# Performance work log

Measured on AMD Instinct MI355X. Metric: run time of the kernel, lower is better.

The kernel has to match this reference:

```python
import jax, jax.numpy as jnp
import numpy as np

N_GAS_NETS = 76  # 29 h2o + 13 o3 + 9 co2 + 3 n2o + 9 ch4 + 13 uniform
N_CHANNELS = 29
N_IN = 2   # (temperature, pressure)
H = 64     # hidden width per n_hidden=[64,64]

# gas index (into composition[0..5]) for each of the 76 stacked nets
COMP_IDX = jnp.asarray(np.repeat(np.arange(6), [29, 13, 9, 3, 9, 13]))

# sparse per-channel combine (hard-coded in the original forward)
H2O_IDX = jnp.asarray([0,1,2,3,4,5,6,3,4,9,10,11,12,13,14,15,16,17,18,19,20,21,22,23,24,25,26,27,28])
O3_CH  = jnp.asarray([0,1,2,17,18,19,20,21,22,25,26,27,28])
CO2_CH = jnp.asarray([0,1,2,5,6,9,10,13,14])
N2O_CH = jnp.asarray([0,1,2])
CH4_CH = jnp.asarray([0,1,2,3,4,7,8,11,12])
U_CH   = jnp.asarray([0,1,2,15,16,17,18,19,20,21,22,27,28])


def setup_inputs() -> dict:
    key = jax.random.key(0)
    ks = jax.random.split(key, 10)
    N = 32768
    t_p = jax.random.normal(ks[0], (N, N_IN), dtype=jnp.float32)
    composition = jax.random.uniform(ks[1], (8, N, 1), dtype=jnp.float32)
    s1 = 1.0 / np.sqrt(N_IN)
    s2 = 1.0 / np.sqrt(H)
    W1 = jax.random.normal(ks[2], (N_GAS_NETS, N_IN, H), dtype=jnp.float32) * s1
    b1 = jnp.zeros((N_GAS_NETS, H), dtype=jnp.float32)
    W2 = jax.random.normal(ks[3], (N_GAS_NETS, H, H), dtype=jnp.float32) * s2
    b2 = jnp.zeros((N_GAS_NETS, H), dtype=jnp.float32)
    Wout = jax.random.normal(ks[4], (N_GAS_NETS, H, 1), dtype=jnp.float32) * s2
    bout = jnp.zeros((N_GAS_NETS, 1), dtype=jnp.float32)
    ke_lw = jax.random.uniform(ks[5], (N_CHANNELS, 1), dtype=jnp.float32)
    ke_iw = jax.random.uniform(ks[6], (N_CHANNELS, 1), dtype=jnp.float32)
    return {"t_p": t_p, "composition": composition, "W1": W1, "b1": b1,
            "W2": W2, "b2": b2, "Wout": Wout, "bout": bout,
            "ke_lw": ke_lw, "ke_iw": ke_iw}


def reference(t_p, composition, W1, b1, W2, b2, Wout, bout, ke_lw, ke_iw):
    # Batched evaluation of all 76 tiny DenseFFN experts on the shared t_p input.
    h = jax.nn.relu(jnp.einsum('ni,gih->gnh', t_p, W1) + b1[:, None, :])   # [76,N,H]
    h = jax.nn.relu(jnp.einsum('gnh,ghk->gnk', h, W2) + b2[:, None, :])    # [76,N,H]
    ke = jax.nn.relu(jnp.einsum('gnh,gho->gno', h, Wout) + bout[:, None, :])  # [76,N,1]

    # tau_gas[gas] = ke * composition[gas_index]
    tau_all = ke * composition[COMP_IDX]  # [76,N,1]
    h2o = tau_all[0:29]
    o3 = tau_all[29:42]
    co2 = tau_all[42:51]
    n2o = tau_all[51:54]
    ch4 = tau_all[54:63]
    u = tau_all[63:76]

    # hard-coded sparse per-channel sum
    tau_gases = h2o[H2O_IDX]                      # [29,N,1]
    tau_gases = tau_gases.at[O3_CH].add(o3)
    tau_gases = tau_gases.at[CO2_CH].add(co2)
    tau_gases = tau_gases.at[N2O_CH].add(n2o)
    tau_gases = tau_gases.at[CH4_CH].add(ch4)
    tau_gases = tau_gases.at[U_CH].add(u)

    tau_lw = ke_lw[:, None, :] * composition[6]   # [29,N,1]
    tau_iw = ke_iw[:, None, :] * composition[7]   # [29,N,1]
    return (tau_gases, tau_lw, tau_iw)
```

## Files before the change

### kernel.cpp

```cpp
#include <hip/hip_runtime.h>

#define NPTS 32768

typedef _Float16 f16;
typedef _Float16 f16x2 __attribute__((ext_vector_type(2)));
typedef _Float16 f16x8 __attribute__((ext_vector_type(8)));
typedef float f32x2 __attribute__((ext_vector_type(2)));
typedef float f32x4 __attribute__((ext_vector_type(4)));
typedef unsigned int u32x4 __attribute__((ext_vector_type(4)));

union U16 { u32x4 u; f32x4 f; f16x2 h2[4]; f16x8 h8; };

static __device__ __forceinline__ f16x2 pk_fma(f16x2 a, f16x2 b, f16x2 c) {
  return __builtin_elementwise_fma(a, b, c);
}
static __device__ __forceinline__ f16x2 pk_relu(f16x2 a) {
  f16x2 z = {(f16)0.f, (f16)0.f};
  return __builtin_elementwise_max(a, z);
}
static __device__ __forceinline__ f16x2 pk_cvt(float a, float b) {
  return __builtin_bit_cast(f16x2, __builtin_amdgcn_cvt_pkrtz(a, b));
}

__device__ const unsigned char G_T[74] = {
  0,0,0,0,0,0,0, 0,0,0,0,0,0,0,0,0,0,0,0,0,0,0,0,0,0,0,0,
  1,1,1,1,1,1,1,1,1,1,1,1,1,
  2,2,2,2,2,2,2,2,2,
  3,3,3,
  4,4,4,4,4,4,4,4,4,
  5,5,5,5,5,5,5,5,5,5,5,5,5
};
__device__ const unsigned char G_C1[74] = {
  0,1,2,3,4,5,6, 9,10,11,12,13,14,15,16,17,18,19,20,21,22,23,24,25,26,27,28,
  0,1,2,17,18,19,20,21,22,25,26,27,28,
  0,1,2,5,6,9,10,13,14,
  0,1,2,
  0,1,2,3,4,7,8,11,12,
  0,1,2,15,16,17,18,19,20,21,22,27,28
};
__device__ const unsigned char G_C2[74] = {
  255,255,255,7,8,255,255, 255,255,255,255,255,255,255,255,255,255,255,255,
  255,255,255,255,255,255,255,255,
  255,255,255,255,255,255,255,255,255,255,255,255,255,
  255,255,255,255,255,255,255,255,255,
  255,255,255,
  255,255,255,255,255,255,255,255,255,
  255,255,255,255,255,255,255,255,255,255,255,255,255
};

#define NSLOT 22

__global__ __launch_bounds__(64) void k0w_pack(
    const float* __restrict__ W1, const float* __restrict__ b1,
    const float* __restrict__ W2, const float* __restrict__ b2,
    const float* __restrict__ Wout, u32x4* __restrict__ pack)
{
  const int gi   = blockIdx.x;
  const int lane = threadIdx.x;
  const int l15  = lane & 15;
  const int quad = lane >> 4;
  const int g    = gi + (gi >= 7 ? 2 : 0);

  const float* W2g = W2 + g * 4096;
  const float* W1g = W1 + g * 128;
  const float* b1g = b1 + g * 64;
  u32x4* dst = pack + gi * NSLOT * 64 + lane;

  #pragma unroll
  for (int mt = 0; mt < 4; ++mt)
    #pragma unroll
    for (int ks = 0; ks < 2; ++ks) {
      U16 u;
      #pragma unroll
      for (int j = 0; j < 4; ++j) {
        const float* s = W2g + (ks * 32 + quad * 8 + 2 * j) * 64 + mt * 16 + l15;
        u.h2[j] = pk_cvt(s[0], s[64]);
      }
      dst[(mt * 2 + ks) * 64] = u.u;
    }
  #pragma unroll
  for (int ks = 0; ks < 2; ++ks) {
    U16 a, b, c;
    #pragma unroll
    for (int j = 0; j < 4; ++j) {
      int h = ks * 32 + quad * 8 + 2 * j;
      a.h2[j] = pk_cvt(W1g[h],      W1g[h + 1]);
      b.h2[j] = pk_cvt(W1g[64 + h], W1g[64 + h + 1]);
      c.h2[j] = pk_cvt(b1g[h],      b1g[h + 1]);
    }
    dst[(8 + ks) * 64]  = a.u;
    dst[(10 + ks) * 64] = b.u;
    dst[(12 + ks) * 64] = c.u;
  }
  #pragma unroll
  for (int mt = 0; mt < 4; ++mt) {
    U16 u, v;
    u.f = *(const f32x4*)(b2   + g * 64 + mt * 16 + quad * 4);
    v.f = *(const f32x4*)(Wout + g * 64 + mt * 16 + quad * 4);
    dst[(14 + mt) * 64] = u.u;
    dst[(18 + mt) * 64] = v.u;
  }
}

__global__ __launch_bounds__(256) void k0_init(
    const float* __restrict__ comp, const float* __restrict__ ke_lw,
    const float* __restrict__ ke_iw, float* __restrict__ out)
{
  const int c = blockIdx.x >> 7;
  const int n = ((blockIdx.x & 127) << 8) + threadIdx.x;
  out[c * NPTS + n] = 0.f;
  out[29 * NPTS + c * NPTS + n] = ke_lw[c] * comp[6 * NPTS + n];
  out[58 * NPTS + c * NPTS + n] = ke_iw[c] * comp[7 * NPTS + n];
}

__global__ __launch_bounds__(256, 2) void k1_mlp(
    const float* __restrict__ t_p, const float* __restrict__ comp,
    const u32x4* __restrict__ pack, const float* __restrict__ bout,
    float* __restrict__ out)
{
  const int lane = threadIdx.x & 63;
  const int l15  = lane & 15;
  const int quad = lane >> 4;
  const int w    = blockIdx.x * 4 + (threadIdx.x >> 6);
  const int gi   = w >> 6;
  const int g    = gi + (gi >= 7 ? 2 : 0);
  const int pb0  = (w & 63) * 512;

  const int t  = G_T[gi];
  const int c1 = G_C1[gi];
  const int c2 = G_C2[gi];

  const bool qb0 = (quad & 1) != 0;
  const bool qb1 = (quad & 2) != 0;

  const u32x4* pksrc = pack + gi * NSLOT * 64 + lane;
  f16x8 afrag[4][2];
  f32x4 b2q[4];
  f32x2 wq2[4][2];
  #pragma unroll
  for (int mt = 0; mt < 4; ++mt) {
    afrag[mt][0] = __builtin_bit_cast(f16x8, pksrc[(mt * 2 + 0) * 64]);
    afrag[mt][1] = __builtin_bit_cast(f16x8, pksrc[(mt * 2 + 1) * 64]);
    b2q[mt] = __builtin_bit_cast(f32x4, pksrc[(14 + mt) * 64]);
    f32x4 wv = __builtin_bit_cast(f32x4, pksrc[(18 + mt) * 64]);
    wq2[mt][0] = f32x2{ wv[0], wv[1] };
    wq2[mt][1] = f32x2{ wv[2], wv[3] };
  }
  U16 w0s[2], w1s[2], b1s[2];
  #pragma unroll
  for (int ks = 0; ks < 2; ++ks) {
    w0s[ks].u = pksrc[(8 + ks) * 64];
    w1s[ks].u = pksrc[(10 + ks) * 64];
    b1s[ks].u = pksrc[(12 + ks) * 64];
  }
  const float bo = bout[g];

  const float2* tp2 = (const float2*)t_p;
  const float* compt = comp + t * NPTS;
  float* out1 = out + c1 * NPTS;
  float* out2 = (c2 == 255) ? nullptr : out + c2 * NPTS;

  float2 xv_n[4];
  float cv_n;
  #pragma unroll
  for (int pt = 0; pt < 4; ++pt)
    xv_n[pt] = tp2[pb0 + pt * 16 + l15];
  cv_n = compt[pb0 + lane];

  #pragma unroll
  for (int pass = 0; pass < 8; ++pass) {
    const int pb = pb0 + pass * 64;

    float2 xv[4];
    #pragma unroll
    for (int pt = 0; pt < 4; ++pt) xv[pt] = xv_n[pt];
    const float cv = cv_n;

    if (pass < 7) {
      const int pbn = pb + 64;
      #pragma unroll
      for (int pt = 0; pt < 4; ++pt)
        xv_n[pt] = tp2[pbn + pt * 16 + l15];
      cv_n = compt[pbn + lane];
    }

    f16x2 x0v[4], x1v[4];
    #pragma unroll
    for (int pt = 0; pt < 4; ++pt) {
      x0v[pt] = pk_cvt(xv[pt].x, xv[pt].x);
      x1v[pt] = pk_cvt(xv[pt].y, xv[pt].y);
    }

    U16 bfrag[2][4];
    #pragma unroll
    for (int ks = 0; ks < 2; ++ks)
      #pragma unroll
      for (int pt = 0; pt < 4; ++pt)
        #pragma unroll
        for (int i = 0; i < 4; ++i)
          bfrag[ks][pt].h2[i] =
              pk_relu(pk_fma(x0v[pt], w0s[ks].h2[i],
                             pk_fma(x1v[pt], w1s[ks].h2[i], b1s[ks].h2[i])));

    f32x2 p2[4];
    #pragma unroll
    for (int pt = 0; pt < 4; ++pt) p2[pt] = f32x2{ 0.f, 0.f };

    #pragma unroll
    for (int mt = 0; mt < 4; ++mt) {
      f32x4 c[4];
      #pragma unroll
      for (int pt = 0; pt < 4; ++pt)
        c[pt] = __builtin_amdgcn_mfma_f32_16x16x32_f16(
            afrag[mt][0], bfrag[0][pt].h8, b2q[mt], 0, 0, 0);
      #pragma unroll
      for (int pt = 0; pt < 4; ++pt)
        c[pt] = __builtin_amdgcn_mfma_f32_16x16x32_f16(
            afrag[mt][1], bfrag[1][pt].h8, c[pt], 0, 0, 0);
      #pragma unroll
      for (int pt = 0; pt < 4; ++pt) {
        f32x2 z = { 0.f, 0.f };
        f32x2 a0 = { c[pt][0], c[pt][1] };
        f32x2 a1 = { c[pt][2], c[pt][3] };
        a0 = __builtin_elementwise_max(a0, z);
        a1 = __builtin_elementwise_max(a1, z);
        p2[pt] = __builtin_elementwise_fma(a0, wq2[mt][0], p2[pt]);
        p2[pt] = __builtin_elementwise_fma(a1, wq2[mt][1], p2[pt]);
      }
    }

    float p[4];
    #pragma unroll
    for (int pt = 0; pt < 4; ++pt) p[pt] = p2[pt][0] + p2[pt][1];

    float u  = qb1 ? (qb0 ? p[3] : p[2]) : (qb0 ? p[1] : p[0]);
    float v  = qb1 ? (qb0 ? p[2] : p[3]) : (qb0 ? p[0] : p[1]);
    float w2 = qb1 ? (qb0 ? p[1] : p[0]) : (qb0 ? p[3] : p[2]);
    float x  = qb1 ? (qb0 ? p[0] : p[1]) : (qb0 ? p[2] : p[3]);
    float s  = u + __shfl_xor(v, 16, 64);
    float tt = w2 + __shfl_xor(x, 16, 64);
    float r  = s + __shfl_xor(tt, 32, 64);

    float tau = fmaxf(r + bo, 0.f) * cv;
    atomicAdd(&out1[pb + lane], tau);
    if (out2) atomicAdd(&out2[pb + lane], tau);
  }
}

extern "C" void kernel_launch(void* const* d_in, const int* in_sizes, int n_in,
                              void* d_out, int out_size, void* d_ws, size_t ws_size,
                              hipStream_t stream)
{
  const float* t_p   = (const float*)d_in[0];
  const float* comp  = (const float*)d_in[1];
  const float* W1    = (const float*)d_in[2];
  const float* b1    = (const float*)d_in[3];
  const float* W2    = (const float*)d_in[4];
  const float* b2    = (const float*)d_in[5];
  const float* Wout  = (const float*)d_in[6];
  const float* bout  = (const float*)d_in[7];
  const float* ke_lw = (const float*)d_in[8];
  const float* ke_iw = (const float*)d_in[9];
  float* out = (float*)d_out;
  u32x4* pack = (u32x4*)d_ws;

  k0w_pack<<<74, 64, 0, stream>>>(W1, b1, W2, b2, Wout, pack);
  k0_init<<<29 * 128, 256, 0, stream>>>(comp, ke_lw, ke_iw, out);
  k1_mlp<<<1184, 256, 0, stream>>>(t_p, comp, pack, bout, out);
}
```

Baseline: 111.4 us.

## Replace atomic channel accumulation with per-net planes and a gather-sum kernel

The MLP kernel now writes each net's tau into its own plane in the workspace instead of atomically adding into output channels. A new gather kernel sums the contributing planes per channel using a static source table and also writes the lw/iw outputs, which replaces the old zero-init kernel. This removes the contended atomics and the separate zeroing pass. In exchange it adds about 9.7 MB of extra plane writes and reads.

```diff
diff --git a/kernel.cpp b/kernel.cpp
--- a/kernel.cpp
+++ b/kernel.cpp
@@ -30,25 +30,28 @@
   4,4,4,4,4,4,4,4,4,
   5,5,5,5,5,5,5,5,5,5,5,5,5
 };
-__device__ const unsigned char G_C1[74] = {
-  0,1,2,3,4,5,6, 9,10,11,12,13,14,15,16,17,18,19,20,21,22,23,24,25,26,27,28,
-  0,1,2,17,18,19,20,21,22,25,26,27,28,
-  0,1,2,5,6,9,10,13,14,
-  0,1,2,
-  0,1,2,3,4,7,8,11,12,
-  0,1,2,15,16,17,18,19,20,21,22,27,28
+
+__device__ const unsigned char CH_SRC[29][6] = {
+  { 0,27,40,49,52,61}, { 1,28,41,50,53,62}, { 2,29,42,51,54,63},
+  { 3,55,255,255,255,255}, { 4,56,255,255,255,255},
+  { 5,43,255,255,255,255}, { 6,44,255,255,255,255},
+  { 3,57,255,255,255,255}, { 4,58,255,255,255,255},
+  { 7,45,255,255,255,255}, { 8,46,255,255,255,255},
+  { 9,59,255,255,255,255}, {10,60,255,255,255,255},
+  {11,47,255,255,255,255}, {12,48,255,255,255,255},
+  {13,64,255,255,255,255}, {14,65,255,255,255,255},
+  {15,30,66,255,255,255}, {16,31,67,255,255,255}, {17,32,68,255,255,255},
+  {18,33,69,255,255,255}, {19,34,70,255,255,255}, {20,35,71,255,255,255},
+  {21,255,255,255,255,255}, {22,255,255,255,255,255},
+  {23,36,255,255,255,255}, {24,37,255,255,255,255},
+  {25,38,72,255,255,255}, {26,39,73,255,255,255}
 };
-__device__ const unsigned char G_C2[74] = {
-  255,255,255,7,8,255,255, 255,255,255,255,255,255,255,255,255,255,255,255,
-  255,255,255,255,255,255,255,255,
-  255,255,255,255,255,255,255,255,255,255,255,255,255,
-  255,255,255,255,255,255,255,255,255,
-  255,255,255,
-  255,255,255,255,255,255,255,255,255,
-  255,255,255,255,255,255,255,255,255,255,255,255,255
+__device__ const unsigned char CH_CNT[29] = {
+  6,6,6, 2,2,2,2,2,2,2,2,2,2,2,2,2,2, 3,3,3,3,3,3, 1,1, 2,2, 3,3
 };
 
 #define NSLOT 22
+#define PACK_SLOTS (74 * NSLOT * 64)
 
 __global__ __launch_bounds__(64) void k0w_pack(
     const float* __restrict__ W1, const float* __restrict__ b1,
@@ -102,21 +105,10 @@
   }
 }
 
-__global__ __launch_bounds__(256) void k0_init(
-    const float* __restrict__ comp, const float* __restrict__ ke_lw,
-    const float* __restrict__ ke_iw, float* __restrict__ out)
-{
-  const int c = blockIdx.x >> 7;
-  const int n = ((blockIdx.x & 127) << 8) + threadIdx.x;
-  out[c * NPTS + n] = 0.f;
-  out[29 * NPTS + c * NPTS + n] = ke_lw[c] * comp[6 * NPTS + n];
-  out[58 * NPTS + c * NPTS + n] = ke_iw[c] * comp[7 * NPTS + n];
-}
-
 __global__ __launch_bounds__(256, 2) void k1_mlp(
     const float* __restrict__ t_p, const float* __restrict__ comp,
     const u32x4* __restrict__ pack, const float* __restrict__ bout,
-    float* __restrict__ out)
+    float* __restrict__ planes)
 {
   const int lane = threadIdx.x & 63;
   const int l15  = lane & 15;
@@ -127,8 +119,6 @@
   const int pb0  = (w & 63) * 512;
 
   const int t  = G_T[gi];
-  const int c1 = G_C1[gi];
-  const int c2 = G_C2[gi];
 
   const bool qb0 = (quad & 1) != 0;
   const bool qb1 = (quad & 2) != 0;
@@ -157,8 +147,7 @@
 
   const float2* tp2 = (const float2*)t_p;
   const float* compt = comp + t * NPTS;
-  float* out1 = out + c1 * NPTS;
-  float* out2 = (c2 == 255) ? nullptr : out + c2 * NPTS;
+  float* plane = planes + gi * NPTS;
 
   float2 xv_n[4];
   float cv_n;
@@ -242,9 +231,28 @@
     float r  = s + __shfl_xor(tt, 32, 64);
 
     float tau = fmaxf(r + bo, 0.f) * cv;
-    atomicAdd(&out1[pb + lane], tau);
-    if (out2) atomicAdd(&out2[pb + lane], tau);
-  }
+    plane[pb + lane] = tau;
+  }
+}
+
+__global__ __launch_bounds__(256) void k2_gather(
+    const float* __restrict__ planes, const float* __restrict__ comp,
+    const float* __restrict__ ke_lw, const float* __restrict__ ke_iw,
+    float* __restrict__ out)
+{
+  const int c  = blockIdx.x >> 5;
+  const int n  = (((blockIdx.x & 31) << 8) + threadIdx.x) * 4;
+
+  const int cnt = CH_CNT[c];
+  f32x4 acc = *(const f32x4*)(planes + (int)CH_SRC[c][0] * NPTS + n);
+  for (int j = 1; j < cnt; ++j)
+    acc += *(const f32x4*)(planes + (int)CH_SRC[c][j] * NPTS + n);
+  *(f32x4*)(out + c * NPTS + n) = acc;
+
+  f32x4 c6 = *(const f32x4*)(comp + 6 * NPTS + n);
+  f32x4 c7 = *(const f32x4*)(comp + 7 * NPTS + n);
+  *(f32x4*)(out + (29 + c) * NPTS + n) = c6 * ke_lw[c];
+  *(f32x4*)(out + (58 + c) * NPTS + n) = c7 * ke_iw[c];
 }
 
 extern "C" void kernel_launch(void* const* d_in, const int* in_sizes, int n_in,
@@ -262,9 +270,11 @@
   const float* ke_lw = (const float*)d_in[8];
   const float* ke_iw = (const float*)d_in[9];
   float* out = (float*)d_out;
-  u32x4* pack = (u32x4*)d_ws;
+
+  u32x4* pack   = (u32x4*)d_ws;
+  float* planes = (float*)(pack + PACK_SLOTS);
 
   k0w_pack<<<74, 64, 0, stream>>>(W1, b1, W2, b2, Wout, pack);
-  k0_init<<<29 * 128, 256, 0, stream>>>(comp, ke_lw, ke_iw, out);
-  k1_mlp<<<1184, 256, 0, stream>>>(t_p, comp, pack, bout, out);
-}
+  k1_mlp<<<1184, 256, 0, stream>>>(t_p, comp, pack, bout, planes);
+  k2_gather<<<29 * 32, 256, 0, stream>>>(planes, comp, ke_lw, ke_iw, out);
+}
```

Result: slower. 117.1 us (+5.1%).
